# Kernel tuning notes

Hardware: AMD Instinct MI355X
Metric: run time of the kernel (lower is better)

Reference implementation:

```python
import jax, jax.numpy as jnp
import numpy as np

B, S, HID = 1, 2048, 4096
NH, KVH, D = 32, 8, 128
MAXP = 2048
EPS = 1e-6


def _rope_tables(max_pos, dim, base=10000.0):
    inv_freq = 1.0 / (base ** (np.arange(0, dim, 2, dtype=np.float32) / dim))
    t = np.arange(max_pos, dtype=np.float32)
    freqs = np.outer(t, inv_freq)                      # [max_pos, dim/2]
    emb = np.concatenate([freqs, freqs], axis=-1)      # [max_pos, dim]
    return jnp.asarray(np.cos(emb)), jnp.asarray(np.sin(emb))


def setup_inputs() -> dict:
    key = jax.random.key(0)
    ks = jax.random.split(key, 6)
    x = jax.random.normal(ks[0], (B, S, HID), jnp.float32)
    scale = 0.02
    wq = jax.random.normal(ks[1], (NH * D, HID), jnp.float32) * scale
    wk = jax.random.normal(ks[2], (KVH * D, HID), jnp.float32) * scale
    wv = jax.random.normal(ks[3], (KVH * D, HID), jnp.float32) * scale
    wo = jax.random.normal(ks[4], (NH * D, HID), jnp.float32).T * scale  # stored as [HID, NH*D] -> transpose back
    wo = jnp.asarray(jax.random.normal(ks[4], (HID, NH * D), jnp.float32) * scale)
    cos_table, sin_table = _rope_tables(MAXP, D)
    return {
        "x": x, "wq": wq, "wk": wk, "wv": wv, "wo": wo,
        "q_norm_w": jnp.ones((D,), jnp.float32),
        "k_norm_w": jnp.ones((D,), jnp.float32),
        "cos_table": cos_table, "sin_table": sin_table,
        "k_cache": jnp.zeros((1, B, MAXP, KVH, D), jnp.float32),
        "v_cache": jnp.zeros((1, B, MAXP, KVH, D), jnp.float32),
        "positions": jnp.arange(S, dtype=jnp.int32),
        "layer_idx": 0,
    }


def _rmsnorm(x, w):
    return w * (x * jax.lax.rsqrt(jnp.mean(x * x, axis=-1, keepdims=True) + EPS))


def _rope(x, cos, sin):
    # x: [B, H, S, D]; cos/sin: [1, 1, S, D]
    half = x.shape[-1] // 2
    x1, x2 = x[..., :half], x[..., half:]
    rotated = jnp.concatenate([-x2, x1], axis=-1)
    return x * cos + rotated * sin


def reference(x, wq, wk, wv, wo, q_norm_w, k_norm_w, cos_table, sin_table,
              k_cache, v_cache, positions, layer_idx):
    bsz, seq_len, _ = x.shape
    d = q_norm_w.shape[0]
    nh = wq.shape[0] // d
    kvh = wk.shape[0] // d
    g = nh // kvh

    q = (x @ wq.T).reshape(bsz, seq_len, nh, d).transpose(0, 2, 1, 3)    # [B,NH,S,D]
    k = (x @ wk.T).reshape(bsz, seq_len, kvh, d).transpose(0, 2, 1, 3)   # [B,KVH,S,D]
    v = (x @ wv.T).reshape(bsz, seq_len, kvh, d).transpose(0, 2, 1, 3)

    q = _rmsnorm(q, q_norm_w)
    k = _rmsnorm(k, k_norm_w)

    cos = cos_table[positions][None, None]  # [1,1,S,D]
    sin = sin_table[positions][None, None]
    q = _rope(q, cos, sin)
    k = _rope(k, cos, sin)

    # KV-cache scatter at dynamic positions (prefill: positions = arange(S))
    kc = k_cache[layer_idx].at[:, positions].set(k.transpose(0, 2, 1, 3))
    vc = v_cache[layer_idx].at[:, positions].set(v.transpose(0, 2, 1, 3))
    # K = max(positions)+1 == seq_len in this (prefill) setup; static for jit
    K = seq_len
    k_all = kc[:, :K].transpose(0, 2, 1, 3)   # [B,KVH,K,D]
    v_all = vc[:, :K].transpose(0, 2, 1, 3)

    # GQA: group query heads instead of repeat_interleave on K/V (same math)
    qg = q.reshape(bsz, kvh, g, seq_len, d)
    scale = 1.0 / jnp.sqrt(jnp.asarray(d, q.dtype))
    scores = jnp.einsum('bkgqd,bkld->bkgql', qg, k_all) * scale
    causal = jnp.tril(jnp.ones((seq_len, K), dtype=bool))
    scores = jnp.where(causal, scores, jnp.finfo(scores.dtype).min)
    attn = jax.nn.softmax(scores, axis=-1)
    out = jnp.einsum('bkgql,bkld->bkgqd', attn, v_all)
    out = out.reshape(bsz, nh, seq_len, d).transpose(0, 2, 1, 3).reshape(bsz, seq_len, nh * d)
    return out @ wo.T
```

## Files before the change

kernel.cpp:

```cpp
#include <hip/hip_runtime.h>

typedef unsigned short u16;
typedef unsigned int u32;
typedef __attribute__((ext_vector_type(8))) short bf16x8;
typedef __attribute__((ext_vector_type(4))) float f32x4;
struct __align__(8) us4 { u16 x, y, z, w; };

#define S_LEN 2048
#define HID   4096
#define NH    32
#define KVH   8
#define HD    128

__device__ inline u16 f2bf(float f) {
  u32 u = __float_as_uint(f);
  u32 r = (u + 0x7fffu + ((u >> 16) & 1u)) >> 16;
  return (u16)r;
}
__device__ inline float bf2f(u16 h) { return __uint_as_float(((u32)h) << 16); }

__device__ inline void gld_lds16(const void* g, void* l) {
  __builtin_amdgcn_global_load_lds(
      (const __attribute__((address_space(1))) u32*)g,
      (__attribute__((address_space(3))) u32*)l, 16, 0, 0);
}

__global__ __launch_bounds__(256)
void cvt_all(const float* __restrict__ x, const float* __restrict__ wq,
             const float* __restrict__ wk, const float* __restrict__ wv,
             const float* __restrict__ wo, u16* __restrict__ xb,
             u16* __restrict__ wqb, u16* __restrict__ wkb,
             u16* __restrict__ wvb, u16* __restrict__ wob) {
  int b = blockIdx.x;
  const float* in; u16* out; int base;
  if (b < 8192)       { in = x;  out = xb;  base = b; }
  else if (b < 24576) { in = wq; out = wqb; base = b - 8192; }
  else if (b < 28672) { in = wk; out = wkb; base = b - 24576; }
  else if (b < 32768) { in = wv; out = wvb; base = b - 28672; }
  else                { in = wo; out = wob; base = b - 32768; }
  size_t i = ((size_t)base * 256 + threadIdx.x) * 4;
  f32x4 v = *(const f32x4*)(in + i);
  us4 o;
  o.x = f2bf(v[0]); o.y = f2bf(v[1]); o.z = f2bf(v[2]); o.w = f2bf(v[3]);
  *(us4*)(out + i) = o;
}

__device__ inline void gemm_core_128(const u16* __restrict__ A,
                                     const u16* __restrict__ W,
                                     int m0, int n0, int K,
                                     int kStart, int kEnd,
                                     u16* lA, u16* lB, f32x4 (&acc)[4][4]) {
  const int t = threadIdx.x;
  const int l = t & 63, w = t >> 6;
  const int quad = l >> 4, l15 = l & 15;
  const int wr = w >> 1, wc = w & 1;
  const int srow = t >> 2;
  const int scol = (t & 3) * 8;
#pragma unroll
  for (int i = 0; i < 4; i++)
#pragma unroll
    for (int j = 0; j < 4; j++) acc[i][j] = (f32x4){0.f, 0.f, 0.f, 0.f};

  for (int k0 = kStart; k0 < kEnd; k0 += 32) {
    gld_lds16(A + (size_t)(m0 + srow) * K + k0 + scol, lA + srow * 32 + scol);
    gld_lds16(A + (size_t)(m0 + 64 + srow) * K + k0 + scol, lA + (64 + srow) * 32 + scol);
    gld_lds16(W + (size_t)(n0 + srow) * K + k0 + scol, lB + srow * 32 + scol);
    gld_lds16(W + (size_t)(n0 + 64 + srow) * K + k0 + scol, lB + (64 + srow) * 32 + scol);
    __syncthreads();
    bf16x8 af[4], bfr[4];
#pragma unroll
    for (int i = 0; i < 4; i++)
      af[i] = *(const bf16x8*)(lA + (wr * 64 + i * 16 + l15) * 32 + quad * 8);
#pragma unroll
    for (int j = 0; j < 4; j++)
      bfr[j] = *(const bf16x8*)(lB + (wc * 64 + j * 16 + l15) * 32 + quad * 8);
#pragma unroll
    for (int i = 0; i < 4; i++)
#pragma unroll
      for (int j = 0; j < 4; j++)
        acc[i][j] = __builtin_amdgcn_mfma_f32_16x16x32_bf16(af[i], bfr[j], acc[i][j], 0, 0, 0);
    __syncthreads();
  }
}

#define QP_ELEMS (S_LEN * HID)
#define KP_ELEMS (S_LEN * 1024)
__global__ __launch_bounds__(256, 3)
void gemm_qkv(const u16* __restrict__ xb, const u16* __restrict__ wqb,
              const u16* __restrict__ wkb, const u16* __restrict__ wvb,
              u16* __restrict__ Qp0, u16* __restrict__ Kp0, u16* __restrict__ vt0) {
  __shared__ __align__(16) u16 lA[128 * 32];
  __shared__ __align__(16) u16 lB[128 * 32];
  const int bx = blockIdx.x;
  const int m0 = blockIdx.y * 128;
  const int z = blockIdx.z;
  const u16* W; u16* C; int n0, ldc, epi;
  if (bx < 32)      { W = wqb; C = Qp0 + (size_t)z * QP_ELEMS; n0 = bx * 128;        ldc = HID;  epi = 0; }
  else if (bx < 40) { W = wkb; C = Kp0 + (size_t)z * KP_ELEMS; n0 = (bx - 32) * 128; ldc = 1024; epi = 0; }
  else              { W = wvb; C = vt0 + (size_t)z * KP_ELEMS; n0 = (bx - 40) * 128; ldc = 0;    epi = 1; }

  f32x4 acc[4][4];
  gemm_core_128(xb, W, m0, n0, HID, z * 2048, z * 2048 + 2048, lA, lB, acc);

  const int t = threadIdx.x, l = t & 63, w = t >> 6;
  const int quad = l >> 4, l15 = l & 15;
  const int wr = w >> 1, wc = w & 1;
  if (epi == 0) {
#pragma unroll
    for (int i = 0; i < 4; i++) {
      int row0 = m0 + wr * 64 + i * 16 + quad * 4;
#pragma unroll
      for (int j = 0; j < 4; j++) {
        int col = n0 + wc * 64 + j * 16 + l15;
#pragma unroll
        for (int r = 0; r < 4; r++)
          C[(size_t)(row0 + r) * ldc + col] = f2bf(acc[i][j][r]);
      }
    }
  } else {
#pragma unroll
    for (int i = 0; i < 4; i++) {
      int row0 = m0 + wr * 64 + i * 16 + quad * 4;
#pragma unroll
      for (int j = 0; j < 4; j++) {
        int col = n0 + wc * 64 + j * 16 + l15;
        us4 v;
        v.x = f2bf(acc[i][j][0]); v.y = f2bf(acc[i][j][1]);
        v.z = f2bf(acc[i][j][2]); v.w = f2bf(acc[i][j][3]);
        *(us4*)(C + (size_t)col * S_LEN + row0) = v;
      }
    }
  }
}

__global__ __launch_bounds__(256, 3)
void gemm_out(const u16* __restrict__ ab, const u16* __restrict__ wob,
              float* __restrict__ O0, float* __restrict__ O1) {
  __shared__ __align__(16) u16 lA[128 * 32];
  __shared__ __align__(16) u16 lB[128 * 32];
  const int m0 = blockIdx.y * 128, n0 = blockIdx.x * 128;
  const int z = blockIdx.z;
  float* Op = z ? O1 : O0;
  f32x4 acc[4][4];
  gemm_core_128(ab, wob, m0, n0, HID, z * 2048, z * 2048 + 2048, lA, lB, acc);
  const int t = threadIdx.x, l = t & 63, w = t >> 6;
  const int quad = l >> 4, l15 = l & 15;
  const int wr = w >> 1, wc = w & 1;
#pragma unroll
  for (int i = 0; i < 4; i++) {
    int row0 = m0 + wr * 64 + i * 16 + quad * 4;
#pragma unroll
    for (int j = 0; j < 4; j++) {
      int col = n0 + wc * 64 + j * 16 + l15;
#pragma unroll
      for (int r = 0; r < 4; r++)
        Op[(size_t)(row0 + r) * HID + col] = acc[i][j][r];
    }
  }
}

__global__ __launch_bounds__(256)
void reduce_out(const float* __restrict__ O0, const float* __restrict__ O1,
                float* __restrict__ outp) {
  size_t i = ((size_t)blockIdx.x * 256 + threadIdx.x) * 4;
  f32x4 a = *(const f32x4*)(O0 + i);
  f32x4 b = *(const f32x4*)(O1 + i);
  a[0] += b[0]; a[1] += b[1]; a[2] += b[2]; a[3] += b[3];
  *(f32x4*)(outp + i) = a;
}

__global__ __launch_bounds__(256)
void rope_all(const u16* __restrict__ Qp0, const u16* __restrict__ Kp0,
              const float* __restrict__ qnw, const float* __restrict__ knw,
              const float* __restrict__ cosT, const float* __restrict__ sinT,
              const int* __restrict__ pos, u16* __restrict__ qbh,
              u16* __restrict__ kbh, const u16* __restrict__ vt0,
              u16* __restrict__ vt) {
  const int b = blockIdx.x;
  const int t = threadIdx.x, w = t >> 6, l = t & 63;
  if (b >= 20480) {
    size_t i = ((size_t)(b - 20480) * 256 + t) * 4;
    us4 a = *(const us4*)(vt0 + i);
    us4 c = *(const us4*)(vt0 + KP_ELEMS + i);
    us4 o;
    o.x = f2bf(bf2f(a.x) + bf2f(c.x)); o.y = f2bf(bf2f(a.y) + bf2f(c.y));
    o.z = f2bf(bf2f(a.z) + bf2f(c.z)); o.w = f2bf(bf2f(a.w) + bf2f(c.w));
    *(us4*)(vt + i) = o;
    return;
  }
  const u16 *xr0, *xr1; const float* nw; u16* orow; int s;
  if (b < 16384) {
    int p = b * 4 + w;
    s = p >> 5; int h = p & 31;
    xr0 = Qp0 + (size_t)s * HID + h * HD;
    xr1 = xr0 + QP_ELEMS;
    nw = qnw;
    orow = qbh + ((size_t)h * S_LEN + s) * HD;
  } else {
    int p = (b - 16384) * 4 + w;
    s = p >> 3; int h = p & 7;
    xr0 = Kp0 + (size_t)s * 1024 + h * HD;
    xr1 = xr0 + KP_ELEMS;
    nw = knw;
    orow = kbh + ((size_t)h * S_LEN + s) * HD;
  }
  float x1 = bf2f(xr0[l]) + bf2f(xr1[l]);
  float x2 = bf2f(xr0[l + 64]) + bf2f(xr1[l + 64]);
  float ss = x1 * x1 + x2 * x2;
#pragma unroll
  for (int m = 1; m < 64; m <<= 1) ss += __shfl_xor(ss, m);
  float rinv = rsqrtf(ss * (1.0f / 128.0f) + 1e-6f);
  float n1 = x1 * rinv * nw[l];
  float n2 = x2 * rinv * nw[l + 64];
  int ps = pos[s];
  float c1 = cosT[ps * HD + l], s1 = sinT[ps * HD + l];
  float c2 = cosT[ps * HD + l + 64], s2 = sinT[ps * HD + l + 64];
  float y1 = n1 * c1 - n2 * s1;
  float y2 = n2 * c2 + n1 * s2;
  orow[l] = f2bf(y1);
  orow[l + 64] = f2bf(y2);
}

__global__ __launch_bounds__(256)
void attn_fwd(const u16* __restrict__ qh, const u16* __restrict__ kbh,
              const u16* __restrict__ vth, u16* __restrict__ ab) {
  __shared__ __align__(16) u16 lK[64 * 128];
  __shared__ __align__(16) u16 lV[128 * 64];
  __shared__ __align__(16) u16 lP[4][16 * 72];
  const int t = threadIdx.x, w = t >> 6, l = t & 63;
  const int quad = l >> 4, l15 = l & 15;
  const int h = blockIdx.x;
  const int qt = 31 - blockIdx.y;
  const int kvh = h >> 2;
  const int q0 = qt * 64;
  const int qrow = q0 + w * 16 + l15;

  bf16x8 qf[4];
#pragma unroll
  for (int ks = 0; ks < 4; ks++)
    qf[ks] = *(const bf16x8*)(qh + ((size_t)h * S_LEN + qrow) * HD + ks * 32 + quad * 8);

  f32x4 accO[8];
#pragma unroll
  for (int j = 0; j < 8; j++) accO[j] = (f32x4){0.f, 0.f, 0.f, 0.f};
  float m_cur = -3.0e38f, l_sum = 0.f;
  const float scale = 0.08838834764831845f;

  const int ntiles = qt + 1;
  for (int tt = 0; tt < ntiles; tt++) {
    const int c0 = tt * 64;
#pragma unroll
    for (int i = 0; i < 4; i++) {
      int Cc = i * 256 + t;
      int r = Cc >> 4, ch = Cc & 15;
      int gch = ch ^ (r & 15);
      gld_lds16(kbh + ((size_t)kvh * S_LEN + c0 + r) * HD + gch * 8, lK + Cc * 8);
    }
#pragma unroll
    for (int i = 0; i < 4; i++) {
      int Cc = i * 256 + t;
      int d = Cc >> 3, ch = Cc & 7;
      int gch = ch ^ (d & 7);
      gld_lds16(vth + ((size_t)kvh * HD + d) * S_LEN + c0 + gch * 8, lV + Cc * 8);
    }
    __syncthreads();

    f32x4 st[4];
#pragma unroll
    for (int i = 0; i < 4; i++) {
      f32x4 sa = (f32x4){0.f, 0.f, 0.f, 0.f};
      int r = i * 16 + l15;
#pragma unroll
      for (int ks = 0; ks < 4; ks++) {
        int lc = ks * 4 + quad;
        bf16x8 kf = *(const bf16x8*)(lK + r * 128 + ((lc ^ (r & 15)) * 8));
        sa = __builtin_amdgcn_mfma_f32_16x16x32_bf16(kf, qf[ks], sa, 0, 0, 0);
      }
      st[i] = sa;
    }

    float tmax = -3.0e38f;
#pragma unroll
    for (int i = 0; i < 4; i++) {
#pragma unroll
      for (int r = 0; r < 4; r++) {
        int kcol = c0 + i * 16 + quad * 4 + r;
        float v = st[i][r] * scale;
        v = (kcol <= qrow) ? v : -3.0e38f;
        st[i][r] = v;
        tmax = fmaxf(tmax, v);
      }
    }
    tmax = fmaxf(tmax, __shfl_xor(tmax, 16));
    tmax = fmaxf(tmax, __shfl_xor(tmax, 32));
    float m_new = fmaxf(m_cur, tmax);
    float alpha = __expf(m_cur - m_new);

    float psum = 0.f;
#pragma unroll
    for (int i = 0; i < 4; i++) {
      us4 pv;
      u16* pp = (u16*)&pv;
#pragma unroll
      for (int r = 0; r < 4; r++) {
        float pe = __expf(st[i][r] - m_new);
        psum += pe;
        pp[r] = f2bf(pe);
      }
      *(us4*)(&lP[w][l15 * 72 + i * 16 + quad * 4]) = pv;
    }
    psum += __shfl_xor(psum, 16);
    psum += __shfl_xor(psum, 32);
    l_sum = l_sum * alpha + psum;
    m_cur = m_new;

#pragma unroll
    for (int r = 0; r < 4; r++) {
      float ar = __shfl(alpha, quad * 4 + r);
#pragma unroll
      for (int j = 0; j < 8; j++) accO[j][r] *= ar;
    }

    bf16x8 pf[2];
#pragma unroll
    for (int ks = 0; ks < 2; ks++)
      pf[ks] = *(const bf16x8*)(&lP[w][l15 * 72 + ks * 32 + quad * 8]);
#pragma unroll
    for (int j = 0; j < 8; j++) {
      int d = j * 16 + l15;
#pragma unroll
      for (int ks = 0; ks < 2; ks++) {
        int lc = ks * 4 + quad;
        bf16x8 vf = *(const bf16x8*)(lV + d * 64 + ((lc ^ (d & 7)) * 8));
        accO[j] = __builtin_amdgcn_mfma_f32_16x16x32_bf16(pf[ks], vf, accO[j], 0, 0, 0);
      }
    }
    __syncthreads();
  }

  float linv = 1.0f / l_sum;
#pragma unroll
  for (int r = 0; r < 4; r++) {
    float lr = __shfl(linv, quad * 4 + r);
    int row = q0 + w * 16 + quad * 4 + r;
#pragma unroll
    for (int j = 0; j < 8; j++) {
      int col = h * HD + j * 16 + l15;
      ab[(size_t)row * HID + col] = f2bf(accO[j][r] * lr);
    }
  }
}

extern "C" void kernel_launch(void* const* d_in, const int* in_sizes, int n_in,
                              void* d_out, int out_size, void* d_ws, size_t ws_size,
                              hipStream_t stream) {
  const float* x    = (const float*)d_in[0];
  const float* wq   = (const float*)d_in[1];
  const float* wk   = (const float*)d_in[2];
  const float* wv   = (const float*)d_in[3];
  const float* wo   = (const float*)d_in[4];
  const float* qnw  = (const float*)d_in[5];
  const float* knw  = (const float*)d_in[6];
  const float* cosT = (const float*)d_in[7];
  const float* sinT = (const float*)d_in[8];
  const int* positions = (const int*)d_in[11];

  char* ws = (char*)d_ws;
  u16* xb  = (u16*)(ws + 0ULL);
  u16* wqb = (u16*)(ws + 16777216ULL);
  u16* wkb = (u16*)(ws + 50331648ULL);
  u16* wvb = (u16*)(ws + 58720256ULL);
  u16* wob = (u16*)(ws + 67108864ULL);
  u16* Qp0 = (u16*)(ws + 100663296ULL);
  u16* Kp0 = (u16*)(ws + 134217728ULL);
  u16* vt0 = (u16*)(ws + 142606336ULL);
  u16* vt  = (u16*)(ws + 150994944ULL);
  u16* qbh = (u16*)(ws + 155189248ULL);
  u16* kbh = (u16*)(ws + 171966464ULL);
  u16* ab  = (u16*)(ws + 176160768ULL);
  float* O0 = (float*)(ws + 16777216ULL);
  float* O1 = (float*)(ws + 100663296ULL);

  cvt_all<<<49152, 256, 0, stream>>>(x, wq, wk, wv, wo, xb, wqb, wkb, wvb, wob);

  gemm_qkv<<<dim3(48, 16, 2), 256, 0, stream>>>(xb, wqb, wkb, wvb, Qp0, Kp0, vt0);

  rope_all<<<22528, 256, 0, stream>>>(Qp0, Kp0, qnw, knw, cosT, sinT, positions,
                                      qbh, kbh, vt0, vt);

  attn_fwd<<<dim3(NH, S_LEN / 64), 256, 0, stream>>>(qbh, kbh, vt, ab);

  gemm_out<<<dim3(HID / 128, S_LEN / 128, 2), 256, 0, stream>>>(ab, wob, O0, O1);
  reduce_out<<<8192, 256, 0, stream>>>(O0, O1, (float*)d_out);
}
```

Baseline: 539.2 us.

## Replace 128x128 GEMMs with 256x256 double-buffered swizzled-LDS 8-wave GEMM core

Rewrites the QKV and output projection GEMMs to use 256x256 tiles with 512 threads, 128KB of dynamic LDS, XOR-swizzled layout and a double-buffered, interleaved load/MFMA pipeline with priority hints. The QKV GEMM drops its split-K, which removes the partial-sum buffers and the V-sum step in rope_all. Block IDs are remapped for L2 locality, and the workspace layout is adjusted. The aim is more data reuse per tile and overlap of global loads with MFMA. The cost is fewer blocks (192 for QKV), which may leave parts of the GPU idle.

```diff
diff --git a/kernel.cpp b/kernel.cpp
--- a/kernel.cpp
+++ b/kernel.cpp
@@ -11,6 +11,7 @@
 #define NH    32
 #define KVH   8
 #define HD    128
+#define MFMA16 __builtin_amdgcn_mfma_f32_16x16x32_bf16
 
 __device__ inline u16 f2bf(float f) {
   u32 u = __float_as_uint(f);
@@ -45,116 +46,209 @@
   *(us4*)(out + i) = o;
 }
 
-__device__ inline void gemm_core_128(const u16* __restrict__ A,
-                                     const u16* __restrict__ W,
-                                     int m0, int n0, int K,
-                                     int kStart, int kEnd,
-                                     u16* lA, u16* lB, f32x4 (&acc)[4][4]) {
+__device__ __forceinline__ void stage_half(const u16* __restrict__ src, int ldk,
+                                           int rowBase, int k0, char* lslot,
+                                           int t) {
+  int rl = t >> 3;
+  int c8 = ((t & 7) ^ (rl & 7)) * 8;
+  gld_lds16(src + (size_t)(rowBase + rl) * ldk + k0 + c8, lslot + t * 16);
+  gld_lds16(src + (size_t)(rowBase + 64 + rl) * ldk + k0 + c8,
+            lslot + 8192 + t * 16);
+}
+
+__device__ __forceinline__ void gemm256_core(
+    const u16* __restrict__ A, const u16* __restrict__ W, int m0, int n0,
+    int ldk, int kBeg, int kEnd, char* lds, f32x4 (&acc)[8][4]) {
   const int t = threadIdx.x;
   const int l = t & 63, w = t >> 6;
-  const int quad = l >> 4, l15 = l & 15;
-  const int wr = w >> 1, wc = w & 1;
-  const int srow = t >> 2;
-  const int scol = (t & 3) * 8;
-#pragma unroll
-  for (int i = 0; i < 4; i++)
-#pragma unroll
-    for (int j = 0; j < 4; j++) acc[i][j] = (f32x4){0.f, 0.f, 0.f, 0.f};
-
-  for (int k0 = kStart; k0 < kEnd; k0 += 32) {
-    gld_lds16(A + (size_t)(m0 + srow) * K + k0 + scol, lA + srow * 32 + scol);
-    gld_lds16(A + (size_t)(m0 + 64 + srow) * K + k0 + scol, lA + (64 + srow) * 32 + scol);
-    gld_lds16(W + (size_t)(n0 + srow) * K + k0 + scol, lB + srow * 32 + scol);
-    gld_lds16(W + (size_t)(n0 + 64 + srow) * K + k0 + scol, lB + (64 + srow) * 32 + scol);
-    __syncthreads();
-    bf16x8 af[4], bfr[4];
-#pragma unroll
-    for (int i = 0; i < 4; i++)
-      af[i] = *(const bf16x8*)(lA + (wr * 64 + i * 16 + l15) * 32 + quad * 8);
-#pragma unroll
-    for (int j = 0; j < 4; j++)
-      bfr[j] = *(const bf16x8*)(lB + (wc * 64 + j * 16 + l15) * 32 + quad * 8);
-#pragma unroll
-    for (int i = 0; i < 4; i++)
-#pragma unroll
-      for (int j = 0; j < 4; j++)
-        acc[i][j] = __builtin_amdgcn_mfma_f32_16x16x32_bf16(af[i], bfr[j], acc[i][j], 0, 0, 0);
-    __syncthreads();
-  }
-}
-
-#define QP_ELEMS (S_LEN * HID)
-#define KP_ELEMS (S_LEN * 1024)
-__global__ __launch_bounds__(256, 3)
-void gemm_qkv(const u16* __restrict__ xb, const u16* __restrict__ wqb,
-              const u16* __restrict__ wkb, const u16* __restrict__ wvb,
-              u16* __restrict__ Qp0, u16* __restrict__ Kp0, u16* __restrict__ vt0) {
-  __shared__ __align__(16) u16 lA[128 * 32];
-  __shared__ __align__(16) u16 lB[128 * 32];
-  const int bx = blockIdx.x;
-  const int m0 = blockIdx.y * 128;
-  const int z = blockIdx.z;
+  const int l15 = l & 15, quad = l >> 4;
+  const int wr = w >> 2, wcn = w & 3;
+  const int nt = (kEnd - kBeg) >> 6;
+  char* ldsA = lds;
+  char* ldsB = lds + 65536;
+  const int swz0 = ((0 + quad) ^ (l15 & 7)) * 16;
+  const int swz1 = ((4 + quad) ^ (l15 & 7)) * 16;
+  const int aB0 = wr * 16384 + l15 * 128;
+  const int bB0 = wcn * 8192 + l15 * 128;
+
+#pragma unroll
+  for (int m = 0; m < 8; m++)
+#pragma unroll
+    for (int n = 0; n < 4; n++) acc[m][n] = (f32x4){0.f, 0.f, 0.f, 0.f};
+
+  stage_half(W, ldk, n0,       kBeg, ldsB,         t);
+  stage_half(A, ldk, m0,       kBeg, ldsA,         t);
+  stage_half(W, ldk, n0 + 128, kBeg, ldsB + 16384, t);
+  stage_half(A, ldk, m0 + 128, kBeg, ldsA + 16384, t);
+  if (nt > 1) {
+    stage_half(W, ldk, n0, kBeg + 64, ldsB + 32768, t);
+    stage_half(A, ldk, m0, kBeg + 64, ldsA + 32768, t);
+    asm volatile("s_waitcnt vmcnt(4)" ::: "memory");
+  } else {
+    asm volatile("s_waitcnt vmcnt(0)" ::: "memory");
+  }
+  __builtin_amdgcn_s_barrier();
+
+  bf16x8 a[4][2], b[2][2], b2[2][2];
+#pragma unroll 1
+  for (int tt = 0; tt < nt; ++tt) {
+    const int d = tt & 1, dn = d ^ 1;
+    const int aO = d * 32768 + aB0;
+    const int bO = d * 32768 + bB0;
+    const int k1 = kBeg + (tt + 1) * 64;
+    const int k2 = k1 + 64;
+
+#pragma unroll
+    for (int m = 0; m < 4; m++) {
+      a[m][0] = *(const bf16x8*)(ldsA + aO + m * 2048 + swz0);
+      a[m][1] = *(const bf16x8*)(ldsA + aO + m * 2048 + swz1);
+    }
+#pragma unroll
+    for (int n = 0; n < 2; n++) {
+      b[n][0] = *(const bf16x8*)(ldsB + bO + n * 2048 + swz0);
+      b[n][1] = *(const bf16x8*)(ldsB + bO + n * 2048 + swz1);
+    }
+    if (tt + 1 < nt) stage_half(W, ldk, n0 + 128, k1, ldsB + dn * 32768 + 16384, t);
+    __builtin_amdgcn_s_barrier();
+    __builtin_amdgcn_s_setprio(1);
+#pragma unroll
+    for (int m = 0; m < 4; m++)
+#pragma unroll
+      for (int n = 0; n < 2; n++) {
+        acc[m][n] = MFMA16(a[m][0], b[n][0], acc[m][n], 0, 0, 0);
+        acc[m][n] = MFMA16(a[m][1], b[n][1], acc[m][n], 0, 0, 0);
+      }
+    __builtin_amdgcn_s_setprio(0);
+    __builtin_amdgcn_s_barrier();
+
+#pragma unroll
+    for (int n = 0; n < 2; n++) {
+      b2[n][0] = *(const bf16x8*)(ldsB + bO + (2 + n) * 2048 + swz0);
+      b2[n][1] = *(const bf16x8*)(ldsB + bO + (2 + n) * 2048 + swz1);
+    }
+    if (tt + 1 < nt) stage_half(A, ldk, m0 + 128, k1, ldsA + dn * 32768 + 16384, t);
+    __builtin_amdgcn_s_barrier();
+    __builtin_amdgcn_s_setprio(1);
+#pragma unroll
+    for (int m = 0; m < 4; m++)
+#pragma unroll
+      for (int n = 0; n < 2; n++) {
+        acc[m][2 + n] = MFMA16(a[m][0], b2[n][0], acc[m][2 + n], 0, 0, 0);
+        acc[m][2 + n] = MFMA16(a[m][1], b2[n][1], acc[m][2 + n], 0, 0, 0);
+      }
+    __builtin_amdgcn_s_setprio(0);
+    __builtin_amdgcn_s_barrier();
+
+#pragma unroll
+    for (int m = 0; m < 4; m++) {
+      a[m][0] = *(const bf16x8*)(ldsA + aO + (4 + m) * 2048 + swz0);
+      a[m][1] = *(const bf16x8*)(ldsA + aO + (4 + m) * 2048 + swz1);
+    }
+    if (tt + 2 < nt) stage_half(W, ldk, n0, k2, ldsB + d * 32768, t);
+    __builtin_amdgcn_s_barrier();
+    __builtin_amdgcn_s_setprio(1);
+#pragma unroll
+    for (int m = 0; m < 4; m++)
+#pragma unroll
+      for (int n = 0; n < 2; n++) {
+        acc[4 + m][n] = MFMA16(a[m][0], b[n][0], acc[4 + m][n], 0, 0, 0);
+        acc[4 + m][n] = MFMA16(a[m][1], b[n][1], acc[4 + m][n], 0, 0, 0);
+      }
+    __builtin_amdgcn_s_setprio(0);
+    __builtin_amdgcn_s_barrier();
+
+    if (tt + 2 < nt) stage_half(A, ldk, m0, k2, ldsA + d * 32768, t);
+    __builtin_amdgcn_s_barrier();
+    __builtin_amdgcn_s_setprio(1);
+#pragma unroll
+    for (int m = 0; m < 4; m++)
+#pragma unroll
+      for (int n = 0; n < 2; n++) {
+        acc[4 + m][2 + n] = MFMA16(a[m][0], b2[n][0], acc[4 + m][2 + n], 0, 0, 0);
+        acc[4 + m][2 + n] = MFMA16(a[m][1], b2[n][1], acc[4 + m][2 + n], 0, 0, 0);
+      }
+    __builtin_amdgcn_s_setprio(0);
+    if (tt + 1 < nt) {
+      if (tt + 2 < nt) asm volatile("s_waitcnt vmcnt(4)" ::: "memory");
+      else             asm volatile("s_waitcnt vmcnt(0)" ::: "memory");
+    }
+    __builtin_amdgcn_s_barrier();
+  }
+}
+
+__global__ __launch_bounds__(512, 2)
+void gemm_qkv8(const u16* __restrict__ xb, const u16* __restrict__ wqb,
+               const u16* __restrict__ wkb, const u16* __restrict__ wvb,
+               u16* __restrict__ Qp, u16* __restrict__ Kp, u16* __restrict__ vt) {
+  extern __shared__ char lds[];
+  const int id = blockIdx.x;
+  const int sw = (id & 7) * 24 + (id >> 3);
+  const int bx = sw % 24, by = sw / 24;
   const u16* W; u16* C; int n0, ldc, epi;
-  if (bx < 32)      { W = wqb; C = Qp0 + (size_t)z * QP_ELEMS; n0 = bx * 128;        ldc = HID;  epi = 0; }
-  else if (bx < 40) { W = wkb; C = Kp0 + (size_t)z * KP_ELEMS; n0 = (bx - 32) * 128; ldc = 1024; epi = 0; }
-  else              { W = wvb; C = vt0 + (size_t)z * KP_ELEMS; n0 = (bx - 40) * 128; ldc = 0;    epi = 1; }
-
-  f32x4 acc[4][4];
-  gemm_core_128(xb, W, m0, n0, HID, z * 2048, z * 2048 + 2048, lA, lB, acc);
+  if (bx < 16)      { W = wqb; C = Qp; n0 = bx * 256;        ldc = HID;  epi = 0; }
+  else if (bx < 20) { W = wkb; C = Kp; n0 = (bx - 16) * 256; ldc = 1024; epi = 0; }
+  else              { W = wvb; C = vt; n0 = (bx - 20) * 256; ldc = 0;    epi = 1; }
+  const int m0 = by * 256;
+
+  f32x4 acc[8][4];
+  gemm256_core(xb, W, m0, n0, HID, 0, HID, lds, acc);
 
   const int t = threadIdx.x, l = t & 63, w = t >> 6;
-  const int quad = l >> 4, l15 = l & 15;
-  const int wr = w >> 1, wc = w & 1;
+  const int l15 = l & 15, quad = l >> 4;
+  const int wr = w >> 2, wcn = w & 3;
   if (epi == 0) {
 #pragma unroll
-    for (int i = 0; i < 4; i++) {
-      int row0 = m0 + wr * 64 + i * 16 + quad * 4;
-#pragma unroll
-      for (int j = 0; j < 4; j++) {
-        int col = n0 + wc * 64 + j * 16 + l15;
+    for (int m = 0; m < 8; m++) {
+      int row0 = m0 + wr * 128 + m * 16 + quad * 4;
+#pragma unroll
+      for (int n = 0; n < 4; n++) {
+        int col = n0 + wcn * 64 + n * 16 + l15;
 #pragma unroll
         for (int r = 0; r < 4; r++)
-          C[(size_t)(row0 + r) * ldc + col] = f2bf(acc[i][j][r]);
+          C[(size_t)(row0 + r) * ldc + col] = f2bf(acc[m][n][r]);
       }
     }
   } else {
 #pragma unroll
-    for (int i = 0; i < 4; i++) {
-      int row0 = m0 + wr * 64 + i * 16 + quad * 4;
-#pragma unroll
-      for (int j = 0; j < 4; j++) {
-        int col = n0 + wc * 64 + j * 16 + l15;
+    for (int m = 0; m < 8; m++) {
+      int row0 = m0 + wr * 128 + m * 16 + quad * 4;
+#pragma unroll
+      for (int n = 0; n < 4; n++) {
+        int col = n0 + wcn * 64 + n * 16 + l15;
         us4 v;
-        v.x = f2bf(acc[i][j][0]); v.y = f2bf(acc[i][j][1]);
-        v.z = f2bf(acc[i][j][2]); v.w = f2bf(acc[i][j][3]);
-        *(us4*)(C + (size_t)col * S_LEN + row0) = v;
-      }
-    }
-  }
-}
-
-__global__ __launch_bounds__(256, 3)
-void gemm_out(const u16* __restrict__ ab, const u16* __restrict__ wob,
-              float* __restrict__ O0, float* __restrict__ O1) {
-  __shared__ __align__(16) u16 lA[128 * 32];
-  __shared__ __align__(16) u16 lB[128 * 32];
-  const int m0 = blockIdx.y * 128, n0 = blockIdx.x * 128;
-  const int z = blockIdx.z;
+        v.x = f2bf(acc[m][n][0]); v.y = f2bf(acc[m][n][1]);
+        v.z = f2bf(acc[m][n][2]); v.w = f2bf(acc[m][n][3]);
+        *(us4*)(vt + (size_t)col * S_LEN + row0) = v;
+      }
+    }
+  }
+}
+
+__global__ __launch_bounds__(512, 2)
+void gemm_out8(const u16* __restrict__ ab, const u16* __restrict__ wob,
+               float* __restrict__ O0, float* __restrict__ O1) {
+  extern __shared__ char lds[];
+  const int id = blockIdx.x;
+  const int sw = (id & 7) * 32 + (id >> 3);
+  const int z = sw >> 7, rem = sw & 127;
+  const int by = rem >> 4, bx = rem & 15;
   float* Op = z ? O1 : O0;
-  f32x4 acc[4][4];
-  gemm_core_128(ab, wob, m0, n0, HID, z * 2048, z * 2048 + 2048, lA, lB, acc);
+
+  f32x4 acc[8][4];
+  gemm256_core(ab, wob, by * 256, bx * 256, HID, z * 2048, z * 2048 + 2048, lds, acc);
+
   const int t = threadIdx.x, l = t & 63, w = t >> 6;
-  const int quad = l >> 4, l15 = l & 15;
-  const int wr = w >> 1, wc = w & 1;
-#pragma unroll
-  for (int i = 0; i < 4; i++) {
-    int row0 = m0 + wr * 64 + i * 16 + quad * 4;
-#pragma unroll
-    for (int j = 0; j < 4; j++) {
-      int col = n0 + wc * 64 + j * 16 + l15;
+  const int l15 = l & 15, quad = l >> 4;
+  const int wr = w >> 2, wcn = w & 3;
+#pragma unroll
+  for (int m = 0; m < 8; m++) {
+    int row0 = by * 256 + wr * 128 + m * 16 + quad * 4;
+#pragma unroll
+    for (int n = 0; n < 4; n++) {
+      int col = bx * 256 + wcn * 64 + n * 16 + l15;
 #pragma unroll
       for (int r = 0; r < 4; r++)
-        Op[(size_t)(row0 + r) * HID + col] = acc[i][j][r];
+        Op[(size_t)(row0 + r) * HID + col] = acc[m][n][r];
     }
   }
 }
@@ -170,42 +264,29 @@
 }
 
 __global__ __launch_bounds__(256)
-void rope_all(const u16* __restrict__ Qp0, const u16* __restrict__ Kp0,
+void rope_all(const u16* __restrict__ Qp, const u16* __restrict__ Kp,
               const float* __restrict__ qnw, const float* __restrict__ knw,
               const float* __restrict__ cosT, const float* __restrict__ sinT,
               const int* __restrict__ pos, u16* __restrict__ qbh,
-              u16* __restrict__ kbh, const u16* __restrict__ vt0,
-              u16* __restrict__ vt) {
+              u16* __restrict__ kbh) {
   const int b = blockIdx.x;
   const int t = threadIdx.x, w = t >> 6, l = t & 63;
-  if (b >= 20480) {
-    size_t i = ((size_t)(b - 20480) * 256 + t) * 4;
-    us4 a = *(const us4*)(vt0 + i);
-    us4 c = *(const us4*)(vt0 + KP_ELEMS + i);
-    us4 o;
-    o.x = f2bf(bf2f(a.x) + bf2f(c.x)); o.y = f2bf(bf2f(a.y) + bf2f(c.y));
-    o.z = f2bf(bf2f(a.z) + bf2f(c.z)); o.w = f2bf(bf2f(a.w) + bf2f(c.w));
-    *(us4*)(vt + i) = o;
-    return;
-  }
-  const u16 *xr0, *xr1; const float* nw; u16* orow; int s;
+  const u16* xr; const float* nw; u16* orow; int s;
   if (b < 16384) {
     int p = b * 4 + w;
     s = p >> 5; int h = p & 31;
-    xr0 = Qp0 + (size_t)s * HID + h * HD;
-    xr1 = xr0 + QP_ELEMS;
+    xr = Qp + (size_t)s * HID + h * HD;
     nw = qnw;
     orow = qbh + ((size_t)h * S_LEN + s) * HD;
   } else {
     int p = (b - 16384) * 4 + w;
     s = p >> 3; int h = p & 7;
-    xr0 = Kp0 + (size_t)s * 1024 + h * HD;
-    xr1 = xr0 + KP_ELEMS;
+    xr = Kp + (size_t)s * 1024 + h * HD;
     nw = knw;
     orow = kbh + ((size_t)h * S_LEN + s) * HD;
   }
-  float x1 = bf2f(xr0[l]) + bf2f(xr1[l]);
-  float x2 = bf2f(xr0[l + 64]) + bf2f(xr1[l + 64]);
+  float x1 = bf2f(xr[l]);
+  float x2 = bf2f(xr[l + 64]);
   float ss = x1 * x1 + x2 * x2;
 #pragma unroll
   for (int m = 1; m < 64; m <<= 1) ss += __shfl_xor(ss, m);
@@ -365,31 +446,39 @@
   const float* sinT = (const float*)d_in[8];
   const int* positions = (const int*)d_in[11];
 
+  static int attr_done = 0;
+  if (!attr_done) {
+    hipFuncSetAttribute((const void*)gemm_qkv8,
+                        hipFuncAttributeMaxDynamicSharedMemorySize, 131072);
+    hipFuncSetAttribute((const void*)gemm_out8,
+                        hipFuncAttributeMaxDynamicSharedMemorySize, 131072);
+    attr_done = 1;
+  }
+
   char* ws = (char*)d_ws;
   u16* xb  = (u16*)(ws + 0ULL);
   u16* wqb = (u16*)(ws + 16777216ULL);
   u16* wkb = (u16*)(ws + 50331648ULL);
   u16* wvb = (u16*)(ws + 58720256ULL);
   u16* wob = (u16*)(ws + 67108864ULL);
-  u16* Qp0 = (u16*)(ws + 100663296ULL);
-  u16* Kp0 = (u16*)(ws + 134217728ULL);
-  u16* vt0 = (u16*)(ws + 142606336ULL);
-  u16* vt  = (u16*)(ws + 150994944ULL);
-  u16* qbh = (u16*)(ws + 155189248ULL);
-  u16* kbh = (u16*)(ws + 171966464ULL);
-  u16* ab  = (u16*)(ws + 176160768ULL);
-  float* O0 = (float*)(ws + 16777216ULL);
-  float* O1 = (float*)(ws + 100663296ULL);
+  u16* Qp  = (u16*)(ws + 100663296ULL);
+  u16* Kp  = (u16*)(ws + 117440512ULL);
+  u16* vt  = (u16*)(ws + 121634816ULL);
+  u16* qbh = (u16*)(ws + 125829120ULL);
+  u16* kbh = (u16*)(ws + 142606336ULL);
+  u16* ab  = (u16*)(ws + 146800640ULL);
+  float* O0 = (float*)(ws + 0ULL);
+  float* O1 = (float*)(ws + 33554432ULL);
 
   cvt_all<<<49152, 256, 0, stream>>>(x, wq, wk, wv, wo, xb, wqb, wkb, wvb, wob);
 
-  gemm_qkv<<<dim3(48, 16, 2), 256, 0, stream>>>(xb, wqb, wkb, wvb, Qp0, Kp0, vt0);
-
-  rope_all<<<22528, 256, 0, stream>>>(Qp0, Kp0, qnw, knw, cosT, sinT, positions,
-                                      qbh, kbh, vt0, vt);
+  gemm_qkv8<<<192, 512, 131072, stream>>>(xb, wqb, wkb, wvb, Qp, Kp, vt);
+
+  rope_all<<<20480, 256, 0, stream>>>(Qp, Kp, qnw, knw, cosT, sinT, positions,
+                                      qbh, kbh);
 
   attn_fwd<<<dim3(NH, S_LEN / 64), 256, 0, stream>>>(qbh, kbh, vt, ab);
 
-  gemm_out<<<dim3(HID / 128, S_LEN / 128, 2), 256, 0, stream>>>(ab, wob, O0, O1);
+  gemm_out8<<<256, 512, 131072, stream>>>(ab, wob, O0, O1);
   reduce_out<<<8192, 256, 0, stream>>>(O0, O1, (float*)d_out);
 }
```

New measurement: 509.5 us. 5.5% less time.
